# Performance work log

Hardware: AMD Instinct MI355X
Metric: run time of the kernel (lower is better)

## Reference

```python
import jax, jax.numpy as jnp
import numpy as np

N = 300000  # occupied voxels
C = 32      # channels
K = 27      # 3x3x3 kernel offsets


def setup_inputs() -> dict:
    key = jax.random.key(0)
    ks = jax.random.split(key, 6)
    x = jax.random.normal(ks[0], (N, C), dtype=jnp.float32)
    # nbr_map[k, i] = index of input voxel that is neighbor of output voxel i at
    # kernel offset k; value N means 'no neighbor' (gathers a zero pad row).
    nbr_map = jax.random.randint(ks[1], (K, N), 0, N + 1, dtype=jnp.int32)
    scale = 1.0 / np.sqrt(K * C)
    w0 = jax.random.normal(ks[2], (K, C, C), dtype=jnp.float32) * scale
    b0 = jax.random.normal(ks[3], (C,), dtype=jnp.float32) * 0.01
    w1 = jax.random.normal(ks[4], (K, C, C), dtype=jnp.float32) * scale
    b1 = jax.random.normal(ks[5], (C,), dtype=jnp.float32) * 0.01
    return {"x": x, "nbr_map": nbr_map, "w0": w0, "b0": b0, "w1": w1, "b1": b1}


def _sparse_conv(feat, w, b, nbr_map):
    # gather (with zero pad row for missing neighbors) -> per-offset GEMM -> sum
    xp = jnp.concatenate([feat, jnp.zeros((1, feat.shape[1]), feat.dtype)], axis=0)
    g = xp[nbr_map]  # [K, N, C]
    return jnp.einsum('knc,kcd->nd', g, w) + b


def reference(x, nbr_map, w0, b0, w1, b1):
    out = jax.nn.relu(_sparse_conv(x, w0, b0, nbr_map))
    out = _sparse_conv(out, w1, b1, nbr_map)
    return out + x  # residual add
```

## Files before the change

kernel.cpp:

```cpp
#include <hip/hip_runtime.h>
#include <hip/hip_bf16.h>

#define NV 300000
#define CH 32
#define KK 27

typedef __attribute__((ext_vector_type(8))) short bf16x8;
typedef __attribute__((ext_vector_type(4))) float f32x4;

#define XB_OFF   0u
#define XB_BYTES 19200128u
#define HB_OFF   19200128u
#define W0T_OFF  38400256u
#define W1T_OFF  38455552u

__device__ __forceinline__ unsigned short f2b(float f) {
    unsigned int u = __builtin_bit_cast(unsigned int, f);
    unsigned int r = (u + 0x7FFFu + ((u >> 16) & 1u)) >> 16;
    return (unsigned short)r;
}

__global__ __launch_bounds__(256) void prep_kernel(
    const float* __restrict__ x,
    const float* __restrict__ w0,
    const float* __restrict__ w1,
    unsigned short* __restrict__ xb,
    unsigned short* __restrict__ hb,
    unsigned short* __restrict__ w0t,
    unsigned short* __restrict__ w1t)
{
    const int NX = NV * CH / 8;
    int tid = blockIdx.x * blockDim.x + threadIdx.x;
    if (tid < NX) {
        int base = tid * 8;
        const float4* p = reinterpret_cast<const float4*>(x + base);
        float4 a = p[0], b = p[1];
        union { unsigned short u[8]; bf16x8 v; } pk;
        pk.u[0] = f2b(a.x); pk.u[1] = f2b(a.y); pk.u[2] = f2b(a.z); pk.u[3] = f2b(a.w);
        pk.u[4] = f2b(b.x); pk.u[5] = f2b(b.y); pk.u[6] = f2b(b.z); pk.u[7] = f2b(b.w);
        *reinterpret_cast<bf16x8*>(xb + base) = pk.v;
        return;
    }
    int t = tid - NX;
    if (t < 4) {
        union { unsigned short u[8]; bf16x8 v; } z; 
        for (int j = 0; j < 8; ++j) z.u[j] = 0;
        *reinterpret_cast<bf16x8*>(xb + NV * CH + t * 8) = z.v;
        return;
    }
    t -= 4;
    if (t < 4) {
        union { unsigned short u[8]; bf16x8 v; } z;
        for (int j = 0; j < 8; ++j) z.u[j] = 0;
        *reinterpret_cast<bf16x8*>(hb + NV * CH + t * 8) = z.v;
        return;
    }
    t -= 4;
    if (t < 2 * KK * CH * CH) {
        int which = t >= KK * CH * CH;
        int e = t - which * KK * CH * CH;
        int k = e / (CH * CH);
        int rem = e - k * (CH * CH);
        int d = rem / CH;
        int c = rem - d * CH;
        const float* w = which ? w1 : w0;
        unsigned short* o = which ? w1t : w0t;
        o[e] = f2b(w[k * CH * CH + c * CH + d]);
    }
}

template <bool FIRST>
__global__ __launch_bounds__(256) void conv_kernel(
    const unsigned short* __restrict__ in_b,
    const int* __restrict__ nbr,
    const unsigned short* __restrict__ wt,
    const float* __restrict__ bias,
    const float* __restrict__ xres,
    unsigned short* __restrict__ out_b,
    float* __restrict__ out_f)
{
    const int wave = (blockIdx.x * blockDim.x + threadIdx.x) >> 6;
    if (wave >= NV / 16) return;
    const int lane = threadIdx.x & 63;
    const int r = lane & 15;
    const int g = lane >> 4;
    const int row0 = wave * 16;
    const int i = row0 + r;

    f32x4 acc0 = {0.f, 0.f, 0.f, 0.f};
    f32x4 acc1 = {0.f, 0.f, 0.f, 0.f};

    const unsigned short* bp0 = wt + r * CH + g * 8;
    const unsigned short* bp1 = wt + (r + 16) * CH + g * 8;

#pragma unroll
    for (int k = 0; k < KK; ++k) {
        int idx = nbr[k * NV + i];
        bf16x8 a  = *reinterpret_cast<const bf16x8*>(in_b + idx * CH + g * 8);
        bf16x8 b0 = *reinterpret_cast<const bf16x8*>(bp0 + k * CH * CH);
        bf16x8 b1 = *reinterpret_cast<const bf16x8*>(bp1 + k * CH * CH);
        acc0 = __builtin_amdgcn_mfma_f32_16x16x32_bf16(a, b0, acc0, 0, 0, 0);
        acc1 = __builtin_amdgcn_mfma_f32_16x16x32_bf16(a, b1, acc1, 0, 0, 0);
    }

    const float bs0 = bias[r];
    const float bs1 = bias[r + 16];
#pragma unroll
    for (int j = 0; j < 4; ++j) {
        int row = row0 + g * 4 + j;
        float v0 = acc0[j] + bs0;
        float v1 = acc1[j] + bs1;
        if (FIRST) {
            v0 = fmaxf(v0, 0.f);
            v1 = fmaxf(v1, 0.f);
            out_b[row * CH + r]      = f2b(v0);
            out_b[row * CH + r + 16] = f2b(v1);
        } else {
            out_f[row * CH + r]      = v0 + xres[row * CH + r];
            out_f[row * CH + r + 16] = v1 + xres[row * CH + r + 16];
        }
    }
}

extern "C" void kernel_launch(void* const* d_in, const int* in_sizes, int n_in,
                              void* d_out, int out_size, void* d_ws, size_t ws_size,
                              hipStream_t stream) {
    const float* x   = (const float*)d_in[0];
    const int* nbr   = (const int*)d_in[1];
    const float* w0  = (const float*)d_in[2];
    const float* b0  = (const float*)d_in[3];
    const float* w1  = (const float*)d_in[4];
    const float* b1  = (const float*)d_in[5];
    float* out = (float*)d_out;

    char* ws = (char*)d_ws;
    unsigned short* xb  = (unsigned short*)(ws + XB_OFF);
    unsigned short* hb  = (unsigned short*)(ws + HB_OFF);
    unsigned short* w0t = (unsigned short*)(ws + W0T_OFF);
    unsigned short* w1t = (unsigned short*)(ws + W1T_OFF);

    {
        int total = NV * CH / 8 + 8 + 2 * KK * CH * CH;
        int blocks = (total + 255) / 256;
        prep_kernel<<<blocks, 256, 0, stream>>>(x, w0, w1, xb, hb, w0t, w1t);
    }
    int waves = NV / 16;
    int blocks = (waves + 3) / 4;
    conv_kernel<true><<<blocks, 256, 0, stream>>>(xb, nbr, w0t, b0, nullptr, hb, nullptr);
    conv_kernel<false><<<blocks, 256, 0, stream>>>(hb, nbr, w1t, b1, x, nullptr, out);
}
```

Before: 264.3 us.

## Process 32 rows per wave and batch neighbor gathers four offsets at a time

Each wave now computes a 32-row output tile instead of 16, so every weight fragment load feeds two MFMA row tiles. The kernel-offset loop is split into groups of four. Each group first issues all index loads, then all gathers, then the MFMAs, which keeps more memory requests in flight per wave. To make the groups divide evenly, the weights are padded to 28 offsets with a zero slice, and the padded offset re-gathers a valid neighbor. The cost is higher register pressure and half as many waves, which could lower occupancy, plus one extra wasted gather and MFMA per group.

Result: no change. 265.4 us (median of 2 runs) (+0.4%).

```diff
diff --git a/kernel.cpp b/kernel.cpp
--- a/kernel.cpp
+++ b/kernel.cpp
@@ -4,15 +4,15 @@
 #define NV 300000
 #define CH 32
 #define KK 27
+#define KP 28
 
 typedef __attribute__((ext_vector_type(8))) short bf16x8;
 typedef __attribute__((ext_vector_type(4))) float f32x4;
 
 #define XB_OFF   0u
-#define XB_BYTES 19200128u
 #define HB_OFF   19200128u
 #define W0T_OFF  38400256u
-#define W1T_OFF  38455552u
+#define W1T_OFF  38457600u
 
 __device__ __forceinline__ unsigned short f2b(float f) {
     unsigned int u = __builtin_bit_cast(unsigned int, f);
@@ -43,7 +43,7 @@
     }
     int t = tid - NX;
     if (t < 4) {
-        union { unsigned short u[8]; bf16x8 v; } z; 
+        union { unsigned short u[8]; bf16x8 v; } z;
         for (int j = 0; j < 8; ++j) z.u[j] = 0;
         *reinterpret_cast<bf16x8*>(xb + NV * CH + t * 8) = z.v;
         return;
@@ -56,16 +56,21 @@
         return;
     }
     t -= 4;
-    if (t < 2 * KK * CH * CH) {
-        int which = t >= KK * CH * CH;
-        int e = t - which * KK * CH * CH;
-        int k = e / (CH * CH);
-        int rem = e - k * (CH * CH);
-        int d = rem / CH;
-        int c = rem - d * CH;
-        const float* w = which ? w1 : w0;
+    const int WELEM = KP * CH * CH;
+    if (t < 2 * WELEM) {
+        int which = t >= WELEM;
+        int e = t - which * WELEM;
+        int k = e >> 10;
+        int rem = e & 1023;
+        int d = rem >> 5;
+        int c = rem & 31;
         unsigned short* o = which ? w1t : w0t;
-        o[e] = f2b(w[k * CH * CH + c * CH + d]);
+        if (k == KK) {
+            o[e] = 0;
+        } else {
+            const float* w = which ? w1 : w0;
+            o[e] = f2b(w[k * 1024 + c * 32 + d]);
+        }
     }
 }
 
@@ -80,44 +85,70 @@
     float* __restrict__ out_f)
 {
     const int wave = (blockIdx.x * blockDim.x + threadIdx.x) >> 6;
-    if (wave >= NV / 16) return;
+    if (wave >= NV / 32) return;
     const int lane = threadIdx.x & 63;
     const int r = lane & 15;
     const int g = lane >> 4;
-    const int row0 = wave * 16;
-    const int i = row0 + r;
+    const int row0 = wave * 32;
+    const int i0 = row0 + r;
+    const int i1 = row0 + 16 + r;
 
-    f32x4 acc0 = {0.f, 0.f, 0.f, 0.f};
-    f32x4 acc1 = {0.f, 0.f, 0.f, 0.f};
+    f32x4 acc00 = {0.f, 0.f, 0.f, 0.f};
+    f32x4 acc01 = {0.f, 0.f, 0.f, 0.f};
+    f32x4 acc10 = {0.f, 0.f, 0.f, 0.f};
+    f32x4 acc11 = {0.f, 0.f, 0.f, 0.f};
 
-    const unsigned short* bp0 = wt + r * CH + g * 8;
-    const unsigned short* bp1 = wt + (r + 16) * CH + g * 8;
+    const unsigned short* wt_r0 = wt + r * CH + g * 8;
+    const unsigned short* wt_r1 = wt + (r + 16) * CH + g * 8;
 
 #pragma unroll
-    for (int k = 0; k < KK; ++k) {
-        int idx = nbr[k * NV + i];
-        bf16x8 a  = *reinterpret_cast<const bf16x8*>(in_b + idx * CH + g * 8);
-        bf16x8 b0 = *reinterpret_cast<const bf16x8*>(bp0 + k * CH * CH);
-        bf16x8 b1 = *reinterpret_cast<const bf16x8*>(bp1 + k * CH * CH);
-        acc0 = __builtin_amdgcn_mfma_f32_16x16x32_bf16(a, b0, acc0, 0, 0, 0);
-        acc1 = __builtin_amdgcn_mfma_f32_16x16x32_bf16(a, b1, acc1, 0, 0, 0);
+    for (int kb = 0; kb < KP; kb += 4) {
+        int idx0[4], idx1[4];
+#pragma unroll
+        for (int j = 0; j < 4; ++j) {
+            int kk = kb + j;
+            int ks = kk < KK ? kk : KK - 1;
+            idx0[j] = nbr[ks * NV + i0];
+            idx1[j] = nbr[ks * NV + i1];
+        }
+        bf16x8 a0[4], a1[4];
+#pragma unroll
+        for (int j = 0; j < 4; ++j) {
+            a0[j] = *reinterpret_cast<const bf16x8*>(in_b + idx0[j] * CH + g * 8);
+            a1[j] = *reinterpret_cast<const bf16x8*>(in_b + idx1[j] * CH + g * 8);
+        }
+#pragma unroll
+        for (int j = 0; j < 4; ++j) {
+            int kk = kb + j;
+            bf16x8 b0 = *reinterpret_cast<const bf16x8*>(wt_r0 + kk * 1024);
+            bf16x8 b1 = *reinterpret_cast<const bf16x8*>(wt_r1 + kk * 1024);
+            acc00 = __builtin_amdgcn_mfma_f32_16x16x32_bf16(a0[j], b0, acc00, 0, 0, 0);
+            acc10 = __builtin_amdgcn_mfma_f32_16x16x32_bf16(a1[j], b0, acc10, 0, 0, 0);
+            acc01 = __builtin_amdgcn_mfma_f32_16x16x32_bf16(a0[j], b1, acc01, 0, 0, 0);
+            acc11 = __builtin_amdgcn_mfma_f32_16x16x32_bf16(a1[j], b1, acc11, 0, 0, 0);
+        }
     }
 
     const float bs0 = bias[r];
     const float bs1 = bias[r + 16];
 #pragma unroll
     for (int j = 0; j < 4; ++j) {
-        int row = row0 + g * 4 + j;
-        float v0 = acc0[j] + bs0;
-        float v1 = acc1[j] + bs1;
+        int ra = row0 + g * 4 + j;
+        int rb = ra + 16;
+        float v00 = acc00[j] + bs0;
+        float v01 = acc01[j] + bs1;
+        float v10 = acc10[j] + bs0;
+        float v11 = acc11[j] + bs1;
         if (FIRST) {
-            v0 = fmaxf(v0, 0.f);
-            v1 = fmaxf(v1, 0.f);
-            out_b[row * CH + r]      = f2b(v0);
-            out_b[row * CH + r + 16] = f2b(v1);
+            out_b[ra * CH + r]      = f2b(fmaxf(v00, 0.f));
+            out_b[ra * CH + r + 16] = f2b(fmaxf(v01, 0.f));
+            out_b[rb * CH + r]      = f2b(fmaxf(v10, 0.f));
+            out_b[rb * CH + r + 16] = f2b(fmaxf(v11, 0.f));
         } else {
-            out_f[row * CH + r]      = v0 + xres[row * CH + r];
-            out_f[row * CH + r + 16] = v1 + xres[row * CH + r + 16];
+            out_f[ra * CH + r]      = v00 + xres[ra * CH + r];
+            out_f[ra * CH + r + 16] = v01 + xres[ra * CH + r + 16];
+            out_f[rb * CH + r]      = v10 + xres[rb * CH + r];
+            out_f[rb * CH + r + 16] = v11 + xres[rb * CH + r + 16];
         }
     }
 }
@@ -140,12 +171,12 @@
     unsigned short* w1t = (unsigned short*)(ws + W1T_OFF);
 
     {
-        int total = NV * CH / 8 + 8 + 2 * KK * CH * CH;
+        int total = NV * CH / 8 + 8 + 2 * KP * CH * CH;
         int blocks = (total + 255) / 256;
         prep_kernel<<<blocks, 256, 0, stream>>>(x, w0, w1, xb, hb, w0t, w1t);
     }
-    int waves = NV / 16;
-    int blocks = (waves + 3) / 4;
+    int threads = (NV / 32) * 64;
+    int blocks = (threads + 255) / 256;
     conv_kernel<true><<<blocks, 256, 0, stream>>>(xb, nbr, w0t, b0, nullptr, hb, nullptr);
     conv_kernel<false><<<blocks, 256, 0, stream>>>(hb, nbr, w1t, b1, x, nullptr, out);
 }
```
